# Optimization experiments

Measured on AMD Instinct MI355X. Metric: run time of the kernel, lower is better.

Reference implementation:

```python
import jax, jax.numpy as jnp
import numpy as np

B, S, C_IN, D, H = 16, 1024, 1280, 512, 8
HD = D // H  # head dim = 64
EPS = 1e-5


def _rope(x):
    # x: [b, h, s, d]; half-split rotation as in the torch module
    d = x.shape[-1]
    half = d // 2
    s = x.shape[2]
    inv_freq = 1.0 / (10000.0 ** (jnp.arange(0, d, 2, dtype=jnp.float32) / d))  # [half]
    ang = jnp.arange(s, dtype=jnp.float32)[:, None] * inv_freq[None, :]  # [s, half]
    sin, cos = jnp.sin(ang), jnp.cos(ang)  # broadcast over [b, h]
    x1, x2 = x[..., :half], x[..., half:]
    return jnp.concatenate([x1 * cos - x2 * sin, x1 * sin + x2 * cos], axis=-1)


def _ln(x, g, b):
    mu = jnp.mean(x, axis=-1, keepdims=True)
    var = jnp.mean((x - mu) ** 2, axis=-1, keepdims=True)
    return (x - mu) * jax.lax.rsqrt(var + EPS) * g + b


def setup_inputs() -> dict:
    key = jax.random.key(0)
    ks = jax.random.split(key, 12)
    def lin(k, fan_in, fan_out):
        lim = 1.0 / np.sqrt(fan_in)
        return jax.random.uniform(k, (fan_in, fan_out), jnp.float32, -lim, lim)
    return {
        "x": jax.random.normal(ks[0], (B, S, C_IN), jnp.float32),
        "w_in": lin(ks[1], C_IN, D), "b_in": jnp.zeros((D,), jnp.float32),
        "w_qkv": lin(ks[2], D, 3 * D), "b_qkv": jnp.zeros((3 * D,), jnp.float32),
        "w_out": lin(ks[3], D, D), "b_out": jnp.zeros((D,), jnp.float32),
        "w_ffn1": lin(ks[4], D, 4 * D), "b_ffn1": jnp.zeros((4 * D,), jnp.float32),
        "w_ffn2": lin(ks[5], 4 * D, D), "b_ffn2": jnp.zeros((D,), jnp.float32),
        "g1": jnp.ones((D,), jnp.float32), "bn1": jnp.zeros((D,), jnp.float32),
        "g2": jnp.ones((D,), jnp.float32), "bn2": jnp.zeros((D,), jnp.float32),
    }


def reference(x, w_in, b_in, w_qkv, b_qkv, w_out, b_out,
              w_ffn1, b_ffn1, w_ffn2, b_ffn2, g1, bn1, g2, bn2):
    h = x @ w_in + b_in  # [b, s, D]
    qkv = (h @ w_qkv + b_qkv).reshape(B, S, 3, H, HD)
    q, k, v = (jnp.transpose(qkv[:, :, i], (0, 2, 1, 3)) for i in range(3))  # [b, h, s, d]
    q, k = _rope(q), _rope(k)
    scores = jnp.einsum('bhqd,bhkd->bhqk', q, k) / np.sqrt(HD)
    attn = jax.nn.softmax(scores, axis=-1)
    o = jnp.einsum('bhqk,bhkd->bhqd', attn, v)
    o = jnp.transpose(o, (0, 2, 1, 3)).reshape(B, S, D)
    o = o @ w_out + b_out
    h = _ln(h + o, g1, bn1)
    ffn = jax.nn.relu(h @ w_ffn1 + b_ffn1) @ w_ffn2 + b_ffn2
    return _ln(h + ffn, g2, bn2)
```

## Files before the change

kernel.cpp:

```cpp
#include <hip/hip_runtime.h>
#include <hip/hip_bf16.h>
#include <math.h>

#define B_   16
#define S_   1024
#define CIN  1280
#define D_   512
#define H_   8
#define HD_  64
#define NROW (B_ * S_)

typedef __bf16 bf16;
typedef float  f32x2  __attribute__((ext_vector_type(2)));
typedef float  f32x4  __attribute__((ext_vector_type(4)));
typedef bf16   bf16x4 __attribute__((ext_vector_type(4)));
typedef bf16   bf16x8 __attribute__((ext_vector_type(8)));

__device__ __forceinline__ void gload_lds16(const bf16* g, bf16* l) {
    __builtin_amdgcn_global_load_lds(
        (const __attribute__((address_space(1))) void*)g,
        (__attribute__((address_space(3))) void*)l, 16, 0, 0);
}

#define SBAR()   __builtin_amdgcn_s_barrier()
#define SCHED0() __builtin_amdgcn_sched_barrier(0)
#define VMCNT8() asm volatile("s_waitcnt vmcnt(8)" ::: "memory")
#define VMCNT2() asm volatile("s_waitcnt vmcnt(2)" ::: "memory")
#define VMCNT0() asm volatile("s_waitcnt vmcnt(0)" ::: "memory")

__device__ __forceinline__ void tr_tile(const float* __restrict__ in,
                                        bf16* __restrict__ out,
                                        int R, int C, int cx, int ry, int t)
{
    __shared__ float T[32][33];
    const int r0 = ry << 5, c0 = cx << 5;
    {
        int lr = t >> 3, lc = (t & 7) << 2;
        f32x4 v = *(const f32x4*)(in + (size_t)(r0 + lr) * C + c0 + lc);
        T[lr][lc] = v[0]; T[lr][lc + 1] = v[1]; T[lr][lc + 2] = v[2]; T[lr][lc + 3] = v[3];
    }
    __syncthreads();
    {
        int oc = t >> 3, orr = (t & 7) << 2;
        bf16x4 o;
        o[0] = (bf16)T[orr][oc];     o[1] = (bf16)T[orr + 1][oc];
        o[2] = (bf16)T[orr + 2][oc]; o[3] = (bf16)T[orr + 3][oc];
        *(bf16x4*)(out + (size_t)(c0 + oc) * R + r0 + orr) = o;
    }
}

#define NCVT (NROW * CIN / 4 / 256)

__global__ __launch_bounds__(256)
void prep_kernel(const float* __restrict__ x, bf16* __restrict__ x_b,
                 const float* __restrict__ w_in,   bf16* __restrict__ win_t,
                 const float* __restrict__ w_qkv,  bf16* __restrict__ wqkv_t,
                 const float* __restrict__ w_out,  bf16* __restrict__ wout_t,
                 const float* __restrict__ w_ffn1, bf16* __restrict__ wf1_t,
                 const float* __restrict__ w_ffn2, bf16* __restrict__ wf2_t,
                 float* __restrict__ cs)
{
    const int t   = threadIdx.x;
    int bid = blockIdx.x;
    if (bid < NCVT) {
        int i = bid * 256 + t;
        f32x4 v = *(const f32x4*)(x + (size_t)i * 4);
        bf16x4 o;
        o[0] = (bf16)v[0]; o[1] = (bf16)v[1]; o[2] = (bf16)v[2]; o[3] = (bf16)v[3];
        *(bf16x4*)(x_b + (size_t)i * 4) = o;
        return;
    }
    bid -= NCVT;
    if (bid < 640)  { tr_tile(w_in,   win_t,  1280, 512,  bid % 16, bid / 16, t); return; }
    bid -= 640;
    if (bid < 768)  { tr_tile(w_qkv,  wqkv_t, 512,  1536, bid % 48, bid / 48, t); return; }
    bid -= 768;
    if (bid < 256)  { tr_tile(w_out,  wout_t, 512,  512,  bid % 16, bid / 16, t); return; }
    bid -= 256;
    if (bid < 1024) { tr_tile(w_ffn1, wf1_t,  512,  2048, bid % 64, bid / 64, t); return; }
    bid -= 1024;
    if (bid < 1024) { tr_tile(w_ffn2, wf2_t,  2048, 512,  bid % 16, bid / 16, t); return; }
    bid -= 1024;
    {
        int idx = bid * 256 + t;
        int s = idx >> 5, i = idx & 31;
        float freq = exp2f(-(float)i * (13.287712379549449f / 32.f));
        float sn, c;
        sincosf((float)s * freq, &sn, &c);
        cs[(size_t)idx * 2]     = c;
        cs[(size_t)idx * 2 + 1] = sn;
    }
}
#define NPREP (NCVT + 640 + 768 + 256 + 1024 + 1024 + 128)

#define ASZ1 (128 * 64)

template<int EPI, bool RELU, bool RES, bool OUTF, bool OUTB>
__global__ __launch_bounds__(256, 2)
void gemm128_kernel(const bf16* __restrict__ A, const bf16* __restrict__ Wt,
                    const float* __restrict__ bias, const bf16* __restrict__ res,
                    float* __restrict__ outf, bf16* __restrict__ outb,
                    const float* __restrict__ cs, bf16* __restrict__ vt,
                    int M, int N, int K)
{
    __shared__ bf16 lds[4 * ASZ1];

    const int tid  = threadIdx.x;
    const int lane = tid & 63;
    const int wid  = tid >> 6;

    const int perX = (M >> 7) >> 3;
    const int lin  = blockIdx.x;
    const int idx  = lin >> 3;
    const int my   = (lin & 7) * perX + (idx & (perX - 1));
    const int nx   = idx / perX;
    const int m0   = my << 7, n0 = nx << 7;

    const int sRow = lane >> 3;
    const int sK   = ((lane & 7) ^ sRow) << 3;

    const int r2  = wid >> 1;
    const int c2  = wid & 1;
    const int cc  = lane & 15;
    const int g   = (lane >> 4) & 3;
    const int swz = (cc & 7) << 4;

    f32x4 acc[4][4] = {};

    auto stage = [&](int t, int b) {
        const bf16* gA = A  + (size_t)m0 * K + t * 64;
        const bf16* gB = Wt + (size_t)n0 * K + t * 64;
        bf16* lA = lds + b * ASZ1;
        bf16* lB = lds + 2 * ASZ1 + b * ASZ1;
        #pragma unroll
        for (int v = 0; v < 4; ++v) {
            const int ch = v * 4 + wid;
            gload_lds16(gA + (size_t)(ch * 8 + sRow) * K + sK, lA + ch * 512);
            gload_lds16(gB + (size_t)(ch * 8 + sRow) * K + sK, lB + ch * 512);
        }
    };

    const int T = K >> 6;
    stage(0, 0);
    stage(1, 1);
    VMCNT8();
    SCHED0();
    SBAR();

    for (int t = 0; t < T; ++t) {
        const int b = t & 1;
        const char* lA = (const char*)(lds + b * ASZ1);
        const char* lB = (const char*)(lds + 2 * ASZ1 + b * ASZ1);

        #pragma unroll
        for (int ks = 0; ks < 2; ++ks) {
            bf16x8 af[4], bfr[4];
            #pragma unroll
            for (int i = 0; i < 4; ++i) {
                const int row = r2 * 64 + i * 16 + cc;
                af[i] = *(const bf16x8*)(lA + row * 128 + ((ks * 64 + g * 16) ^ swz));
            }
            #pragma unroll
            for (int j = 0; j < 4; ++j) {
                const int row = c2 * 64 + j * 16 + cc;
                bfr[j] = *(const bf16x8*)(lB + row * 128 + ((ks * 64 + g * 16) ^ swz));
            }
            __builtin_amdgcn_s_setprio(1);
            #pragma unroll
            for (int i = 0; i < 4; ++i)
                #pragma unroll
                for (int j = 0; j < 4; ++j)
                    acc[i][j] = __builtin_amdgcn_mfma_f32_16x16x32_bf16(af[i], bfr[j], acc[i][j], 0, 0, 0);
            __builtin_amdgcn_s_setprio(0);
        }
        SCHED0();
        SBAR();
        if (t + 2 < T) {
            stage(t + 2, b);
            VMCNT8();
        } else if (t + 1 < T) {
            VMCNT0();
        }
        if (t + 1 < T) { SCHED0(); SBAR(); }
    }

    const int rq = g << 2;
    if constexpr (EPI == 1) {
        const int colb = c2 * 64;
        if (nx < 8) {
            float bj[4];
            #pragma unroll
            for (int j = 0; j < 4; ++j) bj[j] = bias[n0 + colb + j * 16 + cc];
            #pragma unroll
            for (int i = 0; i < 4; ++i) {
                #pragma unroll
                for (int r = 0; r < 4; ++r) {
                    const int gm = m0 + r2 * 64 + i * 16 + rq + r;
                    const int s  = gm & (S_ - 1);
                    #pragma unroll
                    for (int jp = 0; jp < 2; ++jp) {
                        const int d = jp * 16 + cc;
                        f32x2 csv = *(const f32x2*)(cs + ((size_t)s * 32 + d) * 2);
                        float x1 = acc[i][jp][r]     + bj[jp];
                        float x2 = acc[i][jp + 2][r] + bj[jp + 2];
                        const size_t o1 = (size_t)gm * N + n0 + colb + d;
                        outb[o1]      = (bf16)(x1 * csv[0] - x2 * csv[1]);
                        outb[o1 + 32] = (bf16)(x1 * csv[1] + x2 * csv[0]);
                    }
                }
            }
        } else {
            const int col0 = n0 + colb;
            const int hw = (col0 >> 6) & 7;
            const int bb = m0 >> 10;
            bf16* vbase = vt + (size_t)(bb * 8 + hw) * (HD_ * S_);
            const int sb0 = (m0 & (S_ - 1)) + r2 * 64 + rq;
            #pragma unroll
            for (int i = 0; i < 4; ++i) {
                #pragma unroll
                for (int j = 0; j < 4; ++j) {
                    const int d = j * 16 + cc;
                    const float bv = bias[col0 + d];
                    bf16x4 pk;
                    #pragma unroll
                    for (int r = 0; r < 4; ++r) pk[r] = (bf16)(acc[i][j][r] + bv);
                    *(bf16x4*)(vbase + (size_t)d * S_ + sb0 + i * 16) = pk;
                }
            }
        }
    } else {
        #pragma unroll
        for (int i = 0; i < 4; ++i) {
            #pragma unroll
            for (int j = 0; j < 4; ++j) {
                const int gn = n0 + c2 * 64 + j * 16 + cc;
                const float bv = bias[gn];
                #pragma unroll
                for (int r = 0; r < 4; ++r) {
                    const int gm = m0 + r2 * 64 + i * 16 + rq + r;
                    float v = acc[i][j][r] + bv;
                    if (RES)  v += (float)res[(size_t)gm * N + gn];
                    if (RELU) v = fmaxf(v, 0.f);
                    if (OUTF) outf[(size_t)gm * N + gn] = v;
                    if (OUTB) outb[(size_t)gm * N + gn] = (bf16)v;
                }
            }
        }
    }
    (void)cs; (void)vt;
}

#define PST 72

__global__ __launch_bounds__(512)
void attn_kernel(const bf16* __restrict__ qkv, const bf16* __restrict__ vtg,
                 bf16* __restrict__ o)
{
    __shared__ bf16 Ks[3][4096];
    __shared__ bf16 Vs[3][4096];
    __shared__ bf16 Ps[8][16 * PST];

    const int bh  = blockIdx.x;
    const int b   = bh >> 3;
    const int h   = bh & 7;
    const int q0  = blockIdx.y << 7;
    const int tid = threadIdx.x;
    const int lane = tid & 63;
    const int w    = tid >> 6;
    const int c    = lane & 15;
    const int g    = lane >> 4;
    const int swz  = (c & 7) << 4;

    const size_t rs = 3 * D_;
    const bf16* qb = qkv + (size_t)b * S_ * rs + h * HD_;
    const bf16* kb = qb + D_;
    const bf16* vt = vtg + (size_t)bh * HD_ * S_;

    const int sRow = tid >> 3;
    const int sOff = ((tid & 7) ^ (sRow & 7)) << 3;

    bf16x8 qf[2];
    {
        const bf16* qrow = qb + (size_t)(q0 + w * 16 + c) * rs + g * 8;
        qf[0] = *(const bf16x8*)(qrow);
        qf[1] = *(const bf16x8*)(qrow + 32);
    }
    SCHED0();

    bf16x8 vones;
    {
        bf16 one = (bf16)(c == 0 ? 1.f : 0.f);
        #pragma unroll
        for (int u = 0; u < 8; ++u) vones[u] = one;
    }

    auto stage = [&](int t, int buf) {
        gload_lds16(kb + (size_t)(t * 64 + sRow) * rs + sOff, &Ks[buf][0] + (size_t)tid * 8);
        gload_lds16(vt + (size_t)sRow * S_ + t * 64 + sOff,   &Vs[buf][0] + (size_t)tid * 8);
    };

    f32x4 oa[4] = {};
    f32x4 oa5 = {};
    float m_r = -3.0e38f;
    const float CE  = 0.18033688011112042f;
    const float THR = 44.3614195558365f;

    stage(0, 0);
    stage(1, 1);
    VMCNT2();
    SCHED0();
    SBAR();

    for (int t = 0; t < 16; ++t) {
        const int buf = t % 3;
        if (t + 2 < 16) stage(t + 2, (t + 2) % 3);

        const char* kB = (const char*)&Ks[buf][0];
        const char* vB = (const char*)&Vs[buf][0];

        f32x4 sa[4] = {};
        __builtin_amdgcn_s_setprio(1);
        #pragma unroll
        for (int ch = 0; ch < 2; ++ch)
            #pragma unroll
            for (int ks = 0; ks < 4; ++ks) {
                bf16x8 kf = *(const bf16x8*)(kB + (ks * 16 + c) * 128 + ((ch * 64 + g * 16) ^ swz));
                sa[ks] = __builtin_amdgcn_mfma_f32_16x16x32_bf16(kf, qf[ch], sa[ks], 0, 0, 0);
            }
        __builtin_amdgcn_s_setprio(0);

        float pmax = -3.0e38f;
        #pragma unroll
        for (int ks = 0; ks < 4; ++ks)
            pmax = fmaxf(pmax, fmaxf(fmaxf(sa[ks][0], sa[ks][1]), fmaxf(sa[ks][2], sa[ks][3])));
        pmax = fmaxf(pmax, __shfl_xor(pmax, 16, 64));
        pmax = fmaxf(pmax, __shfl_xor(pmax, 32, 64));

        if (!__all(pmax - m_r <= THR)) {
            float mnew = fmaxf(m_r, pmax);
            float sc = __builtin_amdgcn_exp2f((m_r - mnew) * CE);
            #pragma unroll
            for (int r = 0; r < 4; ++r) {
                float scr = __shfl(sc, g * 4 + r, 64);
                #pragma unroll
                for (int j = 0; j < 4; ++j) oa[j][r] *= scr;
                oa5[r] *= scr;
            }
            m_r = mnew;
        }

        const float nmCE = -m_r * CE;
        #pragma unroll
        for (int ks = 0; ks < 4; ++ks) {
            bf16x4 pb;
            #pragma unroll
            for (int r = 0; r < 4; ++r)
                pb[r] = (bf16)__builtin_amdgcn_exp2f(__builtin_fmaf(sa[ks][r], CE, nmCE));
            *(bf16x4*)&Ps[w][c * PST + ks * 16 + g * 4] = pb;
        }

        __builtin_amdgcn_s_setprio(1);
        #pragma unroll
        for (int ch = 0; ch < 2; ++ch) {
            bf16x8 pa = *(const bf16x8*)&Ps[w][c * PST + ch * 32 + g * 8];
            #pragma unroll
            for (int j = 0; j < 4; ++j) {
                bf16x8 vf = *(const bf16x8*)(vB + (j * 16 + c) * 128 + ((ch * 64 + g * 16) ^ swz));
                oa[j] = __builtin_amdgcn_mfma_f32_16x16x32_bf16(pa, vf, oa[j], 0, 0, 0);
            }
            oa5 = __builtin_amdgcn_mfma_f32_16x16x32_bf16(pa, vones, oa5, 0, 0, 0);
        }
        __builtin_amdgcn_s_setprio(0);

        SCHED0();
        if (t + 1 < 16) {
            if (t + 2 < 16) { VMCNT2(); } else { VMCNT0(); }
            SBAR();
        }
    }

    float linv[4];
    #pragma unroll
    for (int r = 0; r < 4; ++r)
        linv[r] = 1.f / __shfl(oa5[r], lane & 48, 64);
    #pragma unroll
    for (int j = 0; j < 4; ++j)
        #pragma unroll
        for (int r = 0; r < 4; ++r) {
            int q = q0 + w * 16 + g * 4 + r;
            o[((size_t)(b * S_) + q) * D_ + h * HD_ + j * 16 + c] = (bf16)(oa[j][r] * linv[r]);
        }
}

template<bool OUTF, bool OUTB>
__global__ __launch_bounds__(256)
void ln_kernel(const bf16* __restrict__ in, const float* __restrict__ g,
               const float* __restrict__ be, float* __restrict__ outf,
               bf16* __restrict__ outb)
{
    const int row  = (blockIdx.x << 2) + (threadIdx.x >> 6);
    const int lane = threadIdx.x & 63;
    const bf16* p = in + (size_t)row * D_ + lane * 8;
    bf16x8 raw = *(const bf16x8*)p;
    float v[8];
    float s = 0.f, s2 = 0.f;
    #pragma unroll
    for (int u = 0; u < 8; ++u) {
        v[u] = (float)raw[u];
        s  += v[u];
        s2 += v[u] * v[u];
    }
    #pragma unroll
    for (int off = 32; off; off >>= 1) {
        s  += __shfl_xor(s,  off, 64);
        s2 += __shfl_xor(s2, off, 64);
    }
    const float mean = s * (1.f / 512.f);
    const float var  = s2 * (1.f / 512.f) - mean * mean;
    const float rstd = rsqrtf(var + 1e-5f);

    f32x4 g0 = *(const f32x4*)(g + lane * 8);
    f32x4 g1 = *(const f32x4*)(g + lane * 8 + 4);
    f32x4 e0 = *(const f32x4*)(be + lane * 8);
    f32x4 e1 = *(const f32x4*)(be + lane * 8 + 4);
    float ov[8];
    #pragma unroll
    for (int u = 0; u < 4; ++u) {
        ov[u]     = (v[u]     - mean) * rstd * g0[u] + e0[u];
        ov[u + 4] = (v[u + 4] - mean) * rstd * g1[u] + e1[u];
    }
    if (OUTF) {
        float* of = outf + (size_t)row * D_ + lane * 8;
        f32x4 o0, o1;
        #pragma unroll
        for (int u = 0; u < 4; ++u) { o0[u] = ov[u]; o1[u] = ov[u + 4]; }
        *(f32x4*)(of)     = o0;
        *(f32x4*)(of + 4) = o1;
    }
    if (OUTB) {
        bf16x8 ob;
        #pragma unroll
        for (int u = 0; u < 8; ++u) ob[u] = (bf16)ov[u];
        *(bf16x8*)(outb + (size_t)row * D_ + lane * 8) = ob;
    }
}

extern "C" void kernel_launch(void* const* d_in, const int* in_sizes, int n_in,
                              void* d_out, int out_size, void* d_ws, size_t ws_size,
                              hipStream_t stream)
{
    const float* x      = (const float*)d_in[0];
    const float* w_in   = (const float*)d_in[1];
    const float* b_in   = (const float*)d_in[2];
    const float* w_qkv  = (const float*)d_in[3];
    const float* b_qkv  = (const float*)d_in[4];
    const float* w_out  = (const float*)d_in[5];
    const float* b_out  = (const float*)d_in[6];
    const float* w_ffn1 = (const float*)d_in[7];
    const float* b_ffn1 = (const float*)d_in[8];
    const float* w_ffn2 = (const float*)d_in[9];
    const float* b_ffn2 = (const float*)d_in[10];
    const float* g1     = (const float*)d_in[11];
    const float* bn1    = (const float*)d_in[12];
    const float* g2     = (const float*)d_in[13];
    const float* bn2    = (const float*)d_in[14];

    char* ws = (char*)d_ws;
    constexpr size_t OFF_XB   = 0;
    constexpr size_t OFF_WIN  = OFF_XB   + 41943040ull;
    constexpr size_t OFF_WQKV = OFF_WIN  + 1310720ull;
    constexpr size_t OFF_WOUT = OFF_WQKV + 1572864ull;
    constexpr size_t OFF_WF1  = OFF_WOUT + 524288ull;
    constexpr size_t OFF_WF2  = OFF_WF1  + 2097152ull;
    constexpr size_t OFF_CS   = OFF_WF2  + 2097152ull;
    constexpr size_t OFF_HB   = OFF_CS   + 33554432ull;
    constexpr size_t OFF_QKV  = OFF_HB   + 16777216ull;
    constexpr size_t OFF_OB   = OFF_QKV  + 50331648ull;
    constexpr size_t OFF_VT   = OFF_OB   + 16777216ull;
    constexpr size_t OFF_H2B  = OFF_VT   + 33554432ull;
    constexpr size_t OFF_F1   = OFF_H2B  + 16777216ull;
    constexpr size_t OFF_T1   = OFF_XB;
    constexpr size_t OFF_T2   = OFF_QKV;

    bf16*  x_b    = (bf16*)(ws + OFF_XB);
    bf16*  win_t  = (bf16*)(ws + OFF_WIN);
    bf16*  wqkv_t = (bf16*)(ws + OFF_WQKV);
    bf16*  wout_t = (bf16*)(ws + OFF_WOUT);
    bf16*  wf1_t  = (bf16*)(ws + OFF_WF1);
    bf16*  wf2_t  = (bf16*)(ws + OFF_WF2);
    float* cs_t   = (float*)(ws + OFF_CS);
    bf16*  h_b    = (bf16*)(ws + OFF_HB);
    bf16*  qkv_b  = (bf16*)(ws + OFF_QKV);
    bf16*  o_b    = (bf16*)(ws + OFF_OB);
    bf16*  vt_g   = (bf16*)(ws + OFF_VT);
    bf16*  h2_b   = (bf16*)(ws + OFF_H2B);
    bf16*  f1_b   = (bf16*)(ws + OFF_F1);
    bf16*  t1_b   = (bf16*)(ws + OFF_T1);
    bf16*  t2_b   = (bf16*)(ws + OFF_T2);

    prep_kernel<<<NPREP, 256, 0, stream>>>(x, x_b, w_in, win_t, w_qkv, wqkv_t,
                                           w_out, wout_t, w_ffn1, wf1_t,
                                           w_ffn2, wf2_t, cs_t);

    gemm128_kernel<0,false,false,false,true><<<(NROW/128) * (D_/128), 256, 0, stream>>>(
        x_b, win_t, b_in, nullptr, nullptr, h_b, nullptr, nullptr, NROW, D_, CIN);
    gemm128_kernel<1,false,false,false,true><<<(NROW/128) * (3*D_/128), 256, 0, stream>>>(
        h_b, wqkv_t, b_qkv, nullptr, nullptr, qkv_b, cs_t, vt_g, NROW, 3*D_, D_);
    attn_kernel<<<dim3(B_*H_, S_/128), 512, 0, stream>>>(qkv_b, vt_g, o_b);
    gemm128_kernel<0,false,true,false,true><<<(NROW/128) * (D_/128), 256, 0, stream>>>(
        o_b, wout_t, b_out, h_b, nullptr, t1_b, nullptr, nullptr, NROW, D_, D_);
    ln_kernel<false,true><<<NROW/4, 256, 0, stream>>>(t1_b, g1, bn1, nullptr, h2_b);
    gemm128_kernel<0,true,false,false,true><<<(NROW/128) * (4*D_/128), 256, 0, stream>>>(
        h2_b, wf1_t, b_ffn1, nullptr, nullptr, f1_b, nullptr, nullptr, NROW, 4*D_, D_);
    gemm128_kernel<0,false,true,false,true><<<(NROW/128) * (D_/128), 256, 0, stream>>>(
        f1_b, wf2_t, b_ffn2, h2_b, nullptr, t2_b, nullptr, nullptr, NROW, D_, 4*D_);
    ln_kernel<true,false><<<NROW/4, 256, 0, stream>>>(t2_b, g2, bn2, (float*)d_out, nullptr);

    (void)in_sizes; (void)n_in; (void)out_size; (void)ws_size;
}
```

Measured before the change: 258.4 us.

## Fuse fp32 input conversion into first GEMM and double-buffer attention K/V

```diff
diff --git a/kernel.cpp b/kernel.cpp
--- a/kernel.cpp
+++ b/kernel.cpp
@@ -25,6 +25,7 @@
 #define SBAR()   __builtin_amdgcn_s_barrier()
 #define SCHED0() __builtin_amdgcn_sched_barrier(0)
 #define VMCNT8() asm volatile("s_waitcnt vmcnt(8)" ::: "memory")
+#define VMCNT4() asm volatile("s_waitcnt vmcnt(4)" ::: "memory")
 #define VMCNT2() asm volatile("s_waitcnt vmcnt(2)" ::: "memory")
 #define VMCNT0() asm volatile("s_waitcnt vmcnt(0)" ::: "memory")
 
@@ -49,11 +50,8 @@
     }
 }
 
-#define NCVT (NROW * CIN / 4 / 256)
-
 __global__ __launch_bounds__(256)
-void prep_kernel(const float* __restrict__ x, bf16* __restrict__ x_b,
-                 const float* __restrict__ w_in,   bf16* __restrict__ win_t,
+void prep_kernel(const float* __restrict__ w_in,   bf16* __restrict__ win_t,
                  const float* __restrict__ w_qkv,  bf16* __restrict__ wqkv_t,
                  const float* __restrict__ w_out,  bf16* __restrict__ wout_t,
                  const float* __restrict__ w_ffn1, bf16* __restrict__ wf1_t,
@@ -62,15 +60,6 @@
 {
     const int t   = threadIdx.x;
     int bid = blockIdx.x;
-    if (bid < NCVT) {
-        int i = bid * 256 + t;
-        f32x4 v = *(const f32x4*)(x + (size_t)i * 4);
-        bf16x4 o;
-        o[0] = (bf16)v[0]; o[1] = (bf16)v[1]; o[2] = (bf16)v[2]; o[3] = (bf16)v[3];
-        *(bf16x4*)(x_b + (size_t)i * 4) = o;
-        return;
-    }
-    bid -= NCVT;
     if (bid < 640)  { tr_tile(w_in,   win_t,  1280, 512,  bid % 16, bid / 16, t); return; }
     bid -= 640;
     if (bid < 768)  { tr_tile(w_qkv,  wqkv_t, 512,  1536, bid % 48, bid / 48, t); return; }
@@ -91,13 +80,13 @@
         cs[(size_t)idx * 2 + 1] = sn;
     }
 }
-#define NPREP (NCVT + 640 + 768 + 256 + 1024 + 1024 + 128)
+#define NPREP (640 + 768 + 256 + 1024 + 1024 + 128)
 
 #define ASZ1 (128 * 64)
 
-template<int EPI, bool RELU, bool RES, bool OUTF, bool OUTB>
+template<int EPI, bool AF32, bool RELU, bool RES, bool OUTF, bool OUTB>
 __global__ __launch_bounds__(256, 2)
-void gemm128_kernel(const bf16* __restrict__ A, const bf16* __restrict__ Wt,
+void gemm128_kernel(const void* __restrict__ Araw, const bf16* __restrict__ Wt,
                     const float* __restrict__ bias, const bf16* __restrict__ res,
                     float* __restrict__ outf, bf16* __restrict__ outb,
                     const float* __restrict__ cs, bf16* __restrict__ vt,
@@ -105,6 +94,9 @@
 {
     __shared__ bf16 lds[4 * ASZ1];
 
+    const bf16*  Ab = (const bf16*)Araw;
+    const float* Af = (const float*)Araw;
+
     const int tid  = threadIdx.x;
     const int lane = tid & 63;
     const int wid  = tid >> 6;
@@ -126,29 +118,70 @@
     const int swz = (cc & 7) << 4;
 
     f32x4 acc[4][4] = {};
-
-    auto stage = [&](int t, int b) {
-        const bf16* gA = A  + (size_t)m0 * K + t * 64;
-        const bf16* gB = Wt + (size_t)n0 * K + t * 64;
+    f32x4 rA[8];
+
+    auto stageA = [&](int t, int b) {
+        const bf16* gA = Ab + (size_t)m0 * K + t * 64;
         bf16* lA = lds + b * ASZ1;
-        bf16* lB = lds + 2 * ASZ1 + b * ASZ1;
         #pragma unroll
         for (int v = 0; v < 4; ++v) {
             const int ch = v * 4 + wid;
             gload_lds16(gA + (size_t)(ch * 8 + sRow) * K + sK, lA + ch * 512);
+        }
+    };
+    auto issueA = [&](int t) {
+        const float* gA = Af + (size_t)m0 * K + t * 64;
+        #pragma unroll
+        for (int v = 0; v < 4; ++v) {
+            const float* p = gA + (size_t)((v * 4 + wid) * 8 + sRow) * K + sK;
+            rA[v * 2]     = *(const f32x4*)(p);
+            rA[v * 2 + 1] = *(const f32x4*)(p + 4);
+        }
+    };
+    auto writeA = [&](int b) {
+        bf16* lA = lds + b * ASZ1;
+        #pragma unroll
+        for (int v = 0; v < 4; ++v) {
+            bf16x8 wv;
+            #pragma unroll
+            for (int u = 0; u < 4; ++u) {
+                wv[u]     = (bf16)rA[v * 2][u];
+                wv[u + 4] = (bf16)rA[v * 2 + 1][u];
+            }
+            *(bf16x8*)(lA + (v * 4 + wid) * 512 + lane * 8) = wv;
+        }
+    };
+    auto stageB = [&](int t, int b) {
+        const bf16* gB = Wt + (size_t)n0 * K + t * 64;
+        bf16* lB = lds + 2 * ASZ1 + b * ASZ1;
+        #pragma unroll
+        for (int v = 0; v < 4; ++v) {
+            const int ch = v * 4 + wid;
             gload_lds16(gB + (size_t)(ch * 8 + sRow) * K + sK, lB + ch * 512);
         }
     };
 
     const int T = K >> 6;
-    stage(0, 0);
-    stage(1, 1);
-    VMCNT8();
+    if constexpr (AF32) {
+        issueA(0); stageB(0, 0);
+        VMCNT4();
+        writeA(0);
+        issueA(1); stageB(1, 1);
+        VMCNT4();
+        writeA(1);
+    } else {
+        stageA(0, 0); stageB(0, 0);
+        stageA(1, 1); stageB(1, 1);
+        VMCNT8();
+    }
     SCHED0();
     SBAR();
 
     for (int t = 0; t < T; ++t) {
         const int b = t & 1;
+        if constexpr (AF32) {
+            if (t + 2 < T) { issueA(t + 2); SCHED0(); }
+        }
         const char* lA = (const char*)(lds + b * ASZ1);
         const char* lB = (const char*)(lds + 2 * ASZ1 + b * ASZ1);
 
@@ -175,11 +208,21 @@
         }
         SCHED0();
         SBAR();
-        if (t + 2 < T) {
-            stage(t + 2, b);
-            VMCNT8();
-        } else if (t + 1 < T) {
-            VMCNT0();
+        if constexpr (AF32) {
+            if (t + 2 < T) {
+                stageB(t + 2, b);
+                VMCNT4();
+                writeA(b);
+            } else if (t + 1 < T) {
+                VMCNT0();
+            }
+        } else {
+            if (t + 2 < T) {
+                stageA(t + 2, b); stageB(t + 2, b);
+                VMCNT8();
+            } else if (t + 1 < T) {
+                VMCNT0();
+            }
         }
         if (t + 1 < T) { SCHED0(); SBAR(); }
     }
@@ -256,8 +299,8 @@
 void attn_kernel(const bf16* __restrict__ qkv, const bf16* __restrict__ vtg,
                  bf16* __restrict__ o)
 {
-    __shared__ bf16 Ks[3][4096];
-    __shared__ bf16 Vs[3][4096];
+    __shared__ bf16 Ks[2][4096];
+    __shared__ bf16 Vs[2][4096];
     __shared__ bf16 Ps[8][16 * PST];
 
     const int bh  = blockIdx.x;
@@ -312,11 +355,9 @@
     SBAR();
 
     for (int t = 0; t < 16; ++t) {
-        const int buf = t % 3;
-        if (t + 2 < 16) stage(t + 2, (t + 2) % 3);
-
-        const char* kB = (const char*)&Ks[buf][0];
-        const char* vB = (const char*)&Vs[buf][0];
+        const int buf = t & 1;
+        const char* kB = (const char*)Ks[buf];
+        const char* vB = (const char*)Vs[buf];
 
         f32x4 sa[4] = {};
         __builtin_amdgcn_s_setprio(1);
@@ -373,10 +414,14 @@
         __builtin_amdgcn_s_setprio(0);
 
         SCHED0();
-        if (t + 1 < 16) {
-            if (t + 2 < 16) { VMCNT2(); } else { VMCNT0(); }
-            SBAR();
-        }
+        SBAR();
+        if (t + 2 < 16) {
+            stage(t + 2, buf);
+            VMCNT2();
+        } else if (t + 1 < 16) {
+            VMCNT0();
+        }
+        if (t + 1 < 16) { SCHED0(); SBAR(); }
     }
 
     float linv[4];
@@ -466,8 +511,8 @@
     const float* bn2    = (const float*)d_in[14];
 
     char* ws = (char*)d_ws;
-    constexpr size_t OFF_XB   = 0;
-    constexpr size_t OFF_WIN  = OFF_XB   + 41943040ull;
+    constexpr size_t OFF_T1   = 0;
+    constexpr size_t OFF_WIN  = OFF_T1   + 41943040ull;
     constexpr size_t OFF_WQKV = OFF_WIN  + 1310720ull;
     constexpr size_t OFF_WOUT = OFF_WQKV + 1572864ull;
     constexpr size_t OFF_WF1  = OFF_WOUT + 524288ull;
@@ -479,10 +524,8 @@
     constexpr size_t OFF_VT   = OFF_OB   + 16777216ull;
     constexpr size_t OFF_H2B  = OFF_VT   + 33554432ull;
     constexpr size_t OFF_F1   = OFF_H2B  + 16777216ull;
-    constexpr size_t OFF_T1   = OFF_XB;
     constexpr size_t OFF_T2   = OFF_QKV;
 
-    bf16*  x_b    = (bf16*)(ws + OFF_XB);
     bf16*  win_t  = (bf16*)(ws + OFF_WIN);
     bf16*  wqkv_t = (bf16*)(ws + OFF_WQKV);
     bf16*  wout_t = (bf16*)(ws + OFF_WOUT);
@@ -498,21 +541,21 @@
     bf16*  t1_b   = (bf16*)(ws + OFF_T1);
     bf16*  t2_b   = (bf16*)(ws + OFF_T2);
 
-    prep_kernel<<<NPREP, 256, 0, stream>>>(x, x_b, w_in, win_t, w_qkv, wqkv_t,
+    prep_kernel<<<NPREP, 256, 0, stream>>>(w_in, win_t, w_qkv, wqkv_t,
                                            w_out, wout_t, w_ffn1, wf1_t,
                                            w_ffn2, wf2_t, cs_t);
 
-    gemm128_kernel<0,false,false,false,true><<<(NROW/128) * (D_/128), 256, 0, stream>>>(
-        x_b, win_t, b_in, nullptr, nullptr, h_b, nullptr, nullptr, NROW, D_, CIN);
-    gemm128_kernel<1,false,false,false,true><<<(NROW/128) * (3*D_/128), 256, 0, stream>>>(
+    gemm128_kernel<0,true,false,false,false,true><<<(NROW/128) * (D_/128), 256, 0, stream>>>(
+        x, win_t, b_in, nullptr, nullptr, h_b, nullptr, nullptr, NROW, D_, CIN);
+    gemm128_kernel<1,false,false,false,false,true><<<(NROW/128) * (3*D_/128), 256, 0, stream>>>(
         h_b, wqkv_t, b_qkv, nullptr, nullptr, qkv_b, cs_t, vt_g, NROW, 3*D_, D_);
     attn_kernel<<<dim3(B_*H_, S_/128), 512, 0, stream>>>(qkv_b, vt_g, o_b);
-    gemm128_kernel<0,false,true,false,true><<<(NROW/128) * (D_/128), 256, 0, stream>>>(
+    gemm128_kernel<0,false,false,true,false,true><<<(NROW/128) * (D_/128), 256, 0, stream>>>(
         o_b, wout_t, b_out, h_b, nullptr, t1_b, nullptr, nullptr, NROW, D_, D_);
     ln_kernel<false,true><<<NROW/4, 256, 0, stream>>>(t1_b, g1, bn1, nullptr, h2_b);
-    gemm128_kernel<0,true,false,false,true><<<(NROW/128) * (4*D_/128), 256, 0, stream>>>(
+    gemm128_kernel<0,false,true,false,false,true><<<(NROW/128) * (4*D_/128), 256, 0, stream>>>(
         h2_b, wf1_t, b_ffn1, nullptr, nullptr, f1_b, nullptr, nullptr, NROW, 4*D_, D_);
-    gemm128_kernel<0,false,true,false,true><<<(NROW/128) * (D_/128), 256, 0, stream>>>(
+    gemm128_kernel<0,false,false,true,false,true><<<(NROW/128) * (D_/128), 256, 0, stream>>>(
         f1_b, wf2_t, b_ffn2, h2_b, nullptr, t2_b, nullptr, nullptr, NROW, D_, 4*D_);
     ln_kernel<true,false><<<NROW/4, 256, 0, stream>>>(t2_b, g2, bn2, (float*)d_out, nullptr);
 
```

Result: no change. 262.7 us (+1.7%).

## Single-buffer GEMM LDS tiles and double-buffer attention K/V staging

Applied to the files above, without the earlier changes.

```diff
diff --git a/kernel.cpp b/kernel.cpp
--- a/kernel.cpp
+++ b/kernel.cpp
@@ -24,7 +24,6 @@
 
 #define SBAR()   __builtin_amdgcn_s_barrier()
 #define SCHED0() __builtin_amdgcn_sched_barrier(0)
-#define VMCNT8() asm volatile("s_waitcnt vmcnt(8)" ::: "memory")
 #define VMCNT2() asm volatile("s_waitcnt vmcnt(2)" ::: "memory")
 #define VMCNT0() asm volatile("s_waitcnt vmcnt(0)" ::: "memory")
 
@@ -103,7 +102,7 @@
                     const float* __restrict__ cs, bf16* __restrict__ vt,
                     int M, int N, int K)
 {
-    __shared__ bf16 lds[4 * ASZ1];
+    __shared__ bf16 lds[2 * ASZ1];
 
     const int tid  = threadIdx.x;
     const int lane = tid & 63;
@@ -127,30 +126,26 @@
 
     f32x4 acc[4][4] = {};
 
-    auto stage = [&](int t, int b) {
+    auto stage = [&](int t) {
         const bf16* gA = A  + (size_t)m0 * K + t * 64;
         const bf16* gB = Wt + (size_t)n0 * K + t * 64;
-        bf16* lA = lds + b * ASZ1;
-        bf16* lB = lds + 2 * ASZ1 + b * ASZ1;
         #pragma unroll
         for (int v = 0; v < 4; ++v) {
             const int ch = v * 4 + wid;
-            gload_lds16(gA + (size_t)(ch * 8 + sRow) * K + sK, lA + ch * 512);
-            gload_lds16(gB + (size_t)(ch * 8 + sRow) * K + sK, lB + ch * 512);
+            gload_lds16(gA + (size_t)(ch * 8 + sRow) * K + sK, lds + ch * 512);
+            gload_lds16(gB + (size_t)(ch * 8 + sRow) * K + sK, lds + ASZ1 + ch * 512);
         }
     };
 
     const int T = K >> 6;
-    stage(0, 0);
-    stage(1, 1);
-    VMCNT8();
+    stage(0);
+    VMCNT0();
     SCHED0();
     SBAR();
 
     for (int t = 0; t < T; ++t) {
-        const int b = t & 1;
-        const char* lA = (const char*)(lds + b * ASZ1);
-        const char* lB = (const char*)(lds + 2 * ASZ1 + b * ASZ1);
+        const char* lA = (const char*)lds;
+        const char* lB = (const char*)(lds + ASZ1);
 
         #pragma unroll
         for (int ks = 0; ks < 2; ++ks) {
@@ -173,15 +168,14 @@
                     acc[i][j] = __builtin_amdgcn_mfma_f32_16x16x32_bf16(af[i], bfr[j], acc[i][j], 0, 0, 0);
             __builtin_amdgcn_s_setprio(0);
         }
-        SCHED0();
-        SBAR();
-        if (t + 2 < T) {
-            stage(t + 2, b);
-            VMCNT8();
-        } else if (t + 1 < T) {
+        if (t + 1 < T) {
+            SCHED0();
+            SBAR();
+            stage(t + 1);
             VMCNT0();
-        }
-        if (t + 1 < T) { SCHED0(); SBAR(); }
+            SCHED0();
+            SBAR();
+        }
     }
 
     const int rq = g << 2;
@@ -256,8 +250,8 @@
 void attn_kernel(const bf16* __restrict__ qkv, const bf16* __restrict__ vtg,
                  bf16* __restrict__ o)
 {
-    __shared__ bf16 Ks[3][4096];
-    __shared__ bf16 Vs[3][4096];
+    __shared__ bf16 Ks[2][4096];
+    __shared__ bf16 Vs[2][4096];
     __shared__ bf16 Ps[8][16 * PST];
 
     const int bh  = blockIdx.x;
@@ -312,11 +306,9 @@
     SBAR();
 
     for (int t = 0; t < 16; ++t) {
-        const int buf = t % 3;
-        if (t + 2 < 16) stage(t + 2, (t + 2) % 3);
-
-        const char* kB = (const char*)&Ks[buf][0];
-        const char* vB = (const char*)&Vs[buf][0];
+        const int buf = t & 1;
+        const char* kB = (const char*)Ks[buf];
+        const char* vB = (const char*)Vs[buf];
 
         f32x4 sa[4] = {};
         __builtin_amdgcn_s_setprio(1);
@@ -373,10 +365,14 @@
         __builtin_amdgcn_s_setprio(0);
 
         SCHED0();
-        if (t + 1 < 16) {
-            if (t + 2 < 16) { VMCNT2(); } else { VMCNT0(); }
-            SBAR();
-        }
+        SBAR();
+        if (t + 2 < 16) {
+            stage(t + 2, buf);
+            VMCNT2();
+        } else if (t + 1 < 16) {
+            VMCNT0();
+        }
+        if (t + 1 < 16) { SCHED0(); SBAR(); }
     }
 
     float linv[4];
```

Result: no change. 263.0 us (+1.8%).

## Stage attention K/V through registers with a single LDS buffer

Applied to the files above, without the earlier changes.

```diff
diff --git a/kernel.cpp b/kernel.cpp
--- a/kernel.cpp
+++ b/kernel.cpp
@@ -25,8 +25,8 @@
 #define SBAR()   __builtin_amdgcn_s_barrier()
 #define SCHED0() __builtin_amdgcn_sched_barrier(0)
 #define VMCNT8() asm volatile("s_waitcnt vmcnt(8)" ::: "memory")
-#define VMCNT2() asm volatile("s_waitcnt vmcnt(2)" ::: "memory")
 #define VMCNT0() asm volatile("s_waitcnt vmcnt(0)" ::: "memory")
+#define LGKM0()  asm volatile("s_waitcnt lgkmcnt(0)" ::: "memory")
 
 __device__ __forceinline__ void tr_tile(const float* __restrict__ in,
                                         bf16* __restrict__ out,
@@ -252,12 +252,12 @@
 
 #define PST 72
 
-__global__ __launch_bounds__(512)
+__global__ __launch_bounds__(512, 8)
 void attn_kernel(const bf16* __restrict__ qkv, const bf16* __restrict__ vtg,
                  bf16* __restrict__ o)
 {
-    __shared__ bf16 Ks[3][4096];
-    __shared__ bf16 Vs[3][4096];
+    __shared__ bf16 Ks[4096];
+    __shared__ bf16 Vs[4096];
     __shared__ bf16 Ps[8][16 * PST];
 
     const int bh  = blockIdx.x;
@@ -285,7 +285,6 @@
         qf[0] = *(const bf16x8*)(qrow);
         qf[1] = *(const bf16x8*)(qrow + 32);
     }
-    SCHED0();
 
     bf16x8 vones;
     {
@@ -294,9 +293,14 @@
         for (int u = 0; u < 8; ++u) vones[u] = one;
     }
 
-    auto stage = [&](int t, int buf) {
-        gload_lds16(kb + (size_t)(t * 64 + sRow) * rs + sOff, &Ks[buf][0] + (size_t)tid * 8);
-        gload_lds16(vt + (size_t)sRow * S_ + t * 64 + sOff,   &Vs[buf][0] + (size_t)tid * 8);
+    bf16x8 kreg, vreg;
+    auto issue = [&](int t) {
+        kreg = *(const bf16x8*)(kb + (size_t)(t * 64 + sRow) * rs + sOff);
+        vreg = *(const bf16x8*)(vt + (size_t)sRow * S_ + t * 64 + sOff);
+    };
+    auto write = [&]() {
+        *(bf16x8*)(&Ks[tid * 8]) = kreg;
+        *(bf16x8*)(&Vs[tid * 8]) = vreg;
     };
 
     f32x4 oa[4] = {};
@@ -305,18 +309,17 @@
     const float CE  = 0.18033688011112042f;
     const float THR = 44.3614195558365f;
 
-    stage(0, 0);
-    stage(1, 1);
-    VMCNT2();
+    issue(0);
     SCHED0();
+    write();
+    issue(1);
+    SCHED0();
+    LGKM0();
     SBAR();
 
     for (int t = 0; t < 16; ++t) {
-        const int buf = t % 3;
-        if (t + 2 < 16) stage(t + 2, (t + 2) % 3);
-
-        const char* kB = (const char*)&Ks[buf][0];
-        const char* vB = (const char*)&Vs[buf][0];
+        const char* kB = (const char*)Ks;
+        const char* vB = (const char*)Vs;
 
         f32x4 sa[4] = {};
         __builtin_amdgcn_s_setprio(1);
@@ -372,9 +375,13 @@
         }
         __builtin_amdgcn_s_setprio(0);
 
-        SCHED0();
         if (t + 1 < 16) {
-            if (t + 2 < 16) { VMCNT2(); } else { VMCNT0(); }
+            SCHED0();
+            SBAR();
+            write();
+            if (t + 2 < 16) issue(t + 2);
+            SCHED0();
+            LGKM0();
             SBAR();
         }
     }
```

New measurement: 349.7 us. +35.3%, slower.
